# Kernel tuning notes

Measured on AMD Instinct MI355X. Metric: run time of the kernel, lower is better.

The kernel has to match this reference:

```python
import jax, jax.numpy as jnp
import numpy as np

B, S, D = 2, 2048, 1024
E, K = 8, 2
H = 1792  # round_up(int(1024*5/3)=1706, 256)


def setup_inputs() -> dict:
    key = jax.random.key(0)
    k1, k2, k3, k4, k5 = jax.random.split(key, 5)
    scale = 0.02
    x = jax.random.normal(k1, (B, S, D), dtype=jnp.float32)
    gate_w = jax.random.normal(k2, (E, D), dtype=jnp.float32) * scale   # nn.Linear(D,E).weight
    w_gate = jax.random.normal(k3, (E, D, H), dtype=jnp.float32) * scale
    w_up = jax.random.normal(k4, (E, D, H), dtype=jnp.float32) * scale
    w_down = jax.random.normal(k5, (E, H, D), dtype=jnp.float32) * scale
    return {"x": x, "gate_w": gate_w, "w_gate": w_gate, "w_up": w_up, "w_down": w_down}


def reference(x, gate_w, w_gate, w_up, w_down):
    b, s, d = x.shape
    x_flat = x.reshape(-1, d)                      # [T, D]
    # Gate computed in bf16 (torch autocast) then cast back to f32.
    logits = (x_flat.astype(jnp.bfloat16) @ gate_w.T.astype(jnp.bfloat16)).astype(jnp.float32)  # [T, E]
    topk_w, topk_idx = jax.lax.top_k(logits, K)    # [T, K]
    topk_w = jax.nn.softmax(topk_w, axis=-1)
    probs = jax.nn.softmax(logits, axis=-1)        # [T, E]
    mean_probs = probs.mean(0)                     # [E]
    load_balance_loss = E * jnp.sum(mean_probs ** 2)
    # Per-token combine weight for each expert (equivalent to sort/split/index_add combine).
    combine = jnp.sum(jax.nn.one_hot(topk_idx, E, dtype=x_flat.dtype) * topk_w[..., None], axis=1)  # [T, E]
    out = jnp.zeros_like(x_flat)
    for e in range(E):  # fixed small expert loop; math identical to grouped dispatch
        g = x_flat @ w_gate[e]                     # [T, H]
        u = x_flat @ w_up[e]                       # [T, H]
        y = (jax.nn.silu(g) * u) @ w_down[e]       # [T, D]
        out = out + y * combine[:, e:e + 1]
    return out.reshape(b, s, d), load_balance_loss, mean_probs
```

## Files before the change

### kernel.cpp

```cpp
#include <hip/hip_runtime.h>
#include <stdint.h>

#define TT 4096
#define DD 1024
#define EE 8
#define HH 1792
#define MP 10240
#define MT256 40
#define MT128 80

typedef __attribute__((ext_vector_type(8))) short short8;
typedef __attribute__((ext_vector_type(4))) short short4v;
typedef __attribute__((ext_vector_type(4))) float f32x4;

static __device__ __forceinline__ unsigned short f2bf(float f) {
  union { float f; uint32_t u; } v; v.f = f;
  return (unsigned short)((v.u + 0x7fffu + ((v.u >> 16) & 1u)) >> 16);
}
static __device__ __forceinline__ float bf2f(unsigned short h) {
  union { uint32_t u; float f; } v; v.u = ((uint32_t)h) << 16;
  return v.f;
}

static __device__ __forceinline__ void gll16(const void* g, const void* l) {
  __builtin_amdgcn_global_load_lds(
      (const __attribute__((address_space(1))) unsigned int*)g,
      (__attribute__((address_space(3))) unsigned int*)l, 16, 0, 0);
}

__global__ __launch_bounds__(256) void prep_weights(
    const float* __restrict__ w_gate, const float* __restrict__ w_up,
    const float* __restrict__ w_down, unsigned short* __restrict__ wguT,
    unsigned short* __restrict__ wdT) {
  __shared__ float L0[64][65];
  __shared__ float L1[64][65];
  const int tid = threadIdx.x;
  const int lr = tid >> 2, lc = (tid & 3) * 16;
  int bid = blockIdx.x;
  if (bid < 3584) {
    const int e = bid / 448, r = bid % 448;
    const int bx = r / 28, by = r % 28;
    const size_t so = (size_t)e * DD * HH + (size_t)(bx * 64) * HH + by * 64;
    const float* g = w_gate + so;
    const float* u = w_up + so;
#pragma unroll
    for (int q = 0; q < 4; ++q) {
      const f32x4 vg = *(const f32x4*)(g + (size_t)lr * HH + lc + 4 * q);
      const f32x4 vu = *(const f32x4*)(u + (size_t)lr * HH + lc + 4 * q);
#pragma unroll
      for (int j = 0; j < 4; ++j) {
        L0[lr][lc + 4 * q + j] = vg[j];
        L1[lr][lc + 4 * q + j] = vu[j];
      }
    }
    __syncthreads();
    unsigned short b0[16], b1[16];
#pragma unroll
    for (int q = 0; q < 16; ++q) {
      b0[q] = f2bf(L0[lc + q][lr]);
      b1[q] = f2bf(L1[lc + q][lr]);
    }
    const int h = by * 64 + lr;
    const int pg = (h >> 4) * 32 + (h & 15);
    unsigned short* dst = wguT + (size_t)e * 2 * HH * DD + (size_t)bx * 64 + lc;
    *(short8*)(dst + (size_t)pg * DD) = *(const short8*)&b0[0];
    *(short8*)(dst + (size_t)pg * DD + 8) = *(const short8*)&b0[8];
    *(short8*)(dst + (size_t)(pg + 16) * DD) = *(const short8*)&b1[0];
    *(short8*)(dst + (size_t)(pg + 16) * DD + 8) = *(const short8*)&b1[8];
  } else {
    bid -= 3584;
    const int e = bid / 448, r = bid % 448;
    const int bx = r / 16, by = r % 16;
    const float* src = w_down + (size_t)e * HH * DD + (size_t)(bx * 64) * DD + by * 64;
#pragma unroll
    for (int q = 0; q < 4; ++q) {
      const f32x4 v = *(const f32x4*)(src + (size_t)lr * DD + lc + 4 * q);
#pragma unroll
      for (int j = 0; j < 4; ++j) L0[lr][lc + 4 * q + j] = v[j];
    }
    __syncthreads();
    unsigned short b0[16];
#pragma unroll
    for (int q = 0; q < 16; ++q) b0[q] = f2bf(L0[lc + q][lr]);
    const int d = by * 64 + lr;
    unsigned short* dst = wdT + (size_t)e * DD * HH + (size_t)d * HH + bx * 64 + lc;
    *(short8*)(dst) = *(const short8*)&b0[0];
    *(short8*)(dst + 8) = *(const short8*)&b0[8];
  }
}

__global__ __launch_bounds__(256) void gate_kernel(
    const float* __restrict__ x, const float* __restrict__ gw,
    float* __restrict__ combine, float* __restrict__ probs, int2* __restrict__ topk) {
  const int lane = threadIdx.x & 63;
  const int wave = threadIdx.x >> 6;
  const int t = blockIdx.x * 4 + wave;
  const float* xr = x + (size_t)t * DD;
  float acc[EE];
#pragma unroll
  for (int e = 0; e < EE; ++e) acc[e] = 0.f;
  for (int i = 0; i < DD / 64; ++i) {
    const int d = i * 64 + lane;
    const float xv = bf2f(f2bf(xr[d]));
#pragma unroll
    for (int e = 0; e < EE; ++e)
      acc[e] += xv * bf2f(f2bf(gw[e * DD + d]));
  }
#pragma unroll
  for (int e = 0; e < EE; ++e) {
#pragma unroll
    for (int off = 32; off > 0; off >>= 1)
      acc[e] += __shfl_xor(acc[e], off, 64);
  }
  if (lane == 0) {
    float lg[EE];
#pragma unroll
    for (int e = 0; e < EE; ++e) lg[e] = bf2f(f2bf(acc[e]));
    float m1 = -1e30f, m2 = -1e30f; int i1 = 0, i2 = 0;
#pragma unroll
    for (int e = 0; e < EE; ++e) {
      const float v = lg[e];
      if (v > m1) { m2 = m1; i2 = i1; m1 = v; i1 = e; }
      else if (v > m2) { m2 = v; i2 = e; }
    }
    const float e2 = expf(m2 - m1);
    const float w1 = 1.f / (1.f + e2);
    const float w2 = e2 * w1;
    float cb[EE];
#pragma unroll
    for (int e = 0; e < EE; ++e) cb[e] = 0.f;
    cb[i1] = w1; cb[i2] += w2;
    float p[EE]; float s = 0.f;
#pragma unroll
    for (int e = 0; e < EE; ++e) { p[e] = expf(lg[e] - m1); s += p[e]; }
    const float inv = 1.f / s;
#pragma unroll
    for (int e = 0; e < EE; ++e) {
      combine[(size_t)t * EE + e] = cb[e];
      probs[(size_t)t * EE + e] = p[e] * inv;
    }
    topk[t] = make_int2(i1, i2);
  }
}

__global__ __launch_bounds__(256) void reduce_kernel(
    const float* __restrict__ probs, float* __restrict__ tail) {
  const int tid = threadIdx.x;
  const int lane = tid & 63, wave = tid >> 6;
  float acc[EE];
#pragma unroll
  for (int e = 0; e < EE; ++e) acc[e] = 0.f;
  for (int t = tid; t < TT; t += 256) {
#pragma unroll
    for (int e = 0; e < EE; ++e) acc[e] += probs[(size_t)t * EE + e];
  }
#pragma unroll
  for (int e = 0; e < EE; ++e) {
#pragma unroll
    for (int off = 32; off > 0; off >>= 1)
      acc[e] += __shfl_xor(acc[e], off, 64);
  }
  __shared__ float sm[4][EE];
  if (lane == 0) {
#pragma unroll
    for (int e = 0; e < EE; ++e) sm[wave][e] = acc[e];
  }
  __syncthreads();
  if (tid == 0) {
    float loss = 0.f;
#pragma unroll
    for (int e = 0; e < EE; ++e) {
      const float m = (sm[0][e] + sm[1][e] + sm[2][e] + sm[3][e]) * (1.f / TT);
      tail[1 + e] = m;
      loss += m * m;
    }
    tail[0] = (float)EE * loss;
  }
}

__global__ __launch_bounds__(512) void route_kernel(
    const int2* __restrict__ topk, const float* __restrict__ combine,
    int* __restrict__ tok_list, float* __restrict__ wt_list,
    int* __restrict__ tab256, int* __restrict__ tab128) {
  const int lane = threadIdx.x & 63;
  const int e = threadIdx.x >> 6;
  __shared__ int cnts[EE], offs[EE];
  int cnt = 0;
  for (int i = 0; i < TT / 64; ++i) {
    const int2 k2 = topk[i * 64 + lane];
    cnt += __popcll(__ballot(k2.x == e || k2.y == e));
  }
  if (lane == 0) cnts[e] = cnt;
  __syncthreads();
  if (threadIdx.x == 0) {
    int off = 0, n256 = 0, n128 = 0;
    for (int f = 0; f < EE; ++f) {
      offs[f] = off;
      const int pc = (cnts[f] + 255) & ~255;
      for (int j = 0; j < (pc >> 8); ++j) {
        tab256[2 * n256] = f; tab256[2 * n256 + 1] = off + 256 * j; ++n256;
      }
      for (int j = 0; j < (pc >> 7); ++j) {
        tab128[2 * n128] = f; tab128[2 * n128 + 1] = off + 128 * j; ++n128;
      }
      off += pc;
    }
    for (; n256 < MT256; ++n256) { tab256[2 * n256] = -1; tab256[2 * n256 + 1] = 0; }
    for (; n128 < MT128; ++n128) { tab128[2 * n128] = -1; tab128[2 * n128 + 1] = 0; }
  }
  __syncthreads();
  int pos = offs[e];
  for (int i = 0; i < TT / 64; ++i) {
    const int t = i * 64 + lane;
    const int2 k2 = topk[t];
    const bool sel = (k2.x == e || k2.y == e);
    const unsigned long long m = __ballot(sel);
    if (sel) {
      const int p = pos + __popcll(m & ((1ull << lane) - 1ull));
      tok_list[p] = t;
      wt_list[p] = combine[(size_t)t * EE + e];
    }
    pos += __popcll(m);
  }
  const int pc = (cnt + 255) & ~255;
  for (int s = cnt + lane; s < pc; s += 64) {
    tok_list[offs[e] + s] = 0;
    wt_list[offs[e] + s] = 0.f;
  }
}

__global__ __launch_bounds__(256) void gather_x(
    const float* __restrict__ x, const int* __restrict__ tok_list,
    const int* __restrict__ tab256, unsigned short* __restrict__ xg) {
  const int e = tab256[2 * blockIdx.x];
  if (e < 0) return;
  const int row0 = tab256[2 * blockIdx.x + 1] + blockIdx.y * 16;
  const int tid = threadIdx.x;
#pragma unroll
  for (int i = 0; i < 16; ++i) {
    const int row = row0 + i;
    const int tok = tok_list[row];
    const f32x4 v = *(const f32x4*)(x + (size_t)tok * DD + tid * 4);
    unsigned short b[4] = {f2bf(v[0]), f2bf(v[1]), f2bf(v[2]), f2bf(v[3])};
    *(short4v*)(xg + (size_t)row * DD + tid * 4) = *(const short4v*)b;
  }
}

template <int MODE>
__global__ __launch_bounds__(256, 3) void gemm128(
    const unsigned short* __restrict__ Ab, const unsigned short* __restrict__ Bb,
    const int* __restrict__ tab, const int* __restrict__ tok_list,
    const float* __restrict__ wt_list, unsigned short* __restrict__ act,
    float* __restrict__ out) {
  constexpr int K   = (MODE == 0) ? DD : HH;
  constexpr int NBR = (MODE == 0) ? 2 * HH : DD;
  constexpr int NNT = NBR / 128;
  __shared__ unsigned short As[128 * 64];
  __shared__ unsigned short Bs[128 * 64];

  const int nwg = gridDim.x;
  const int wgid = (blockIdx.x & 7) * (nwg >> 3) + (blockIdx.x >> 3);
  const int mt = wgid / NNT, nt = wgid % NNT;
  const int e = tab[2 * mt];
  if (e < 0) return;
  const int row0 = tab[2 * mt + 1];
  const int n0 = nt * 128;

  const int tid = threadIdx.x, lane = tid & 63, wave = tid >> 6;
  const int wm = (wave >> 1) * 64, wn = (wave & 1) * 64;
  const int fr = lane & 15, hi = lane >> 4;

  const unsigned short* At = Ab + (size_t)row0 * K;
  const unsigned short* Bt = Bb + ((size_t)e * NBR + n0) * K;

  const int srel = tid * 16;
  const int srow0 = srel >> 7;
  const int sch = (srel >> 4) & 7;

  f32x4 acc[4][4];
#pragma unroll
  for (int i = 0; i < 4; ++i)
#pragma unroll
    for (int j = 0; j < 4; ++j) acc[i][j] = (f32x4){0.f, 0.f, 0.f, 0.f};

  for (int k0 = 0; k0 < K; k0 += 64) {
#pragma unroll
    for (int q = 0; q < 4; ++q) {
      const int row = q * 32 + srow0;
      gll16(At + (size_t)row * K + k0 + ((sch ^ (row & 7)) << 3),
            (const char*)As + q * 4096 + srel);
    }
#pragma unroll
    for (int q = 0; q < 4; ++q) {
      const int row = q * 32 + srow0;
      gll16(Bt + (size_t)row * K + k0 + ((sch ^ (row & 7)) << 3),
            (const char*)Bs + q * 4096 + srel);
    }
    __syncthreads();
#pragma unroll
    for (int kc = 0; kc < 2; ++kc) {
      short8 a[4], b[4];
#pragma unroll
      for (int i = 0; i < 4; ++i) {
        const int row = wm + i * 16 + fr;
        a[i] = *(const short8*)((const char*)As + ((row * 128 + kc * 64 + hi * 16) ^ ((row & 7) << 4)));
      }
#pragma unroll
      for (int j = 0; j < 4; ++j) {
        const int row = wn + j * 16 + fr;
        b[j] = *(const short8*)((const char*)Bs + ((row * 128 + kc * 64 + hi * 16) ^ ((row & 7) << 4)));
      }
#pragma unroll
      for (int i = 0; i < 4; ++i)
#pragma unroll
        for (int j = 0; j < 4; ++j)
          acc[i][j] = __builtin_amdgcn_mfma_f32_16x16x32_bf16(a[i], b[j], acc[i][j], 0, 0, 0);
    }
    __syncthreads();
  }

  const int r4 = hi * 4;
  if constexpr (MODE == 0) {
#pragma unroll
    for (int i = 0; i < 4; ++i)
#pragma unroll
      for (int r = 0; r < 4; ++r) {
        const int row = row0 + wm + i * 16 + r4 + r;
#pragma unroll
        for (int jj = 0; jj < 2; ++jj) {
          const float g = acc[i][2 * jj][r], u = acc[i][2 * jj + 1][r];
          const int nb = n0 + wn + jj * 32;
          const int h = ((nb >> 5) << 4) + fr;
          act[(size_t)row * HH + h] = f2bf((g / (1.f + expf(-g))) * u);
        }
      }
  } else {
#pragma unroll
    for (int i = 0; i < 4; ++i)
#pragma unroll
      for (int r = 0; r < 4; ++r) {
        const int rl = row0 + wm + i * 16 + r4 + r;
        const int tok = tok_list[rl];
        const float wt = wt_list[rl];
        if (wt != 0.f) {
#pragma unroll
          for (int j = 0; j < 4; ++j)
            unsafeAtomicAdd(&out[(size_t)tok * DD + n0 + wn + j * 16 + fr],
                            acc[i][j][r] * wt);
        }
      }
  }
}

extern "C" void kernel_launch(void* const* d_in, const int* in_sizes, int n_in,
                              void* d_out, int out_size, void* d_ws, size_t ws_size,
                              hipStream_t stream) {
  const float* x      = (const float*)d_in[0];
  const float* gw     = (const float*)d_in[1];
  const float* w_gate = (const float*)d_in[2];
  const float* w_up   = (const float*)d_in[3];
  const float* w_down = (const float*)d_in[4];
  float* out = (float*)d_out;
  float* tail = out + (size_t)TT * DD;

  char* w = (char*)d_ws;
  size_t o = 0;
  auto carve = [&](size_t bytes) { char* p = w + o; o += (bytes + 255) & ~255ull; return p; };
  unsigned short* wguT = (unsigned short*)carve((size_t)EE * 2 * HH * DD * 2);
  unsigned short* wdT  = (unsigned short*)carve((size_t)EE * DD * HH * 2);
  unsigned short* xg   = (unsigned short*)carve((size_t)MP * DD * 2);
  unsigned short* act  = (unsigned short*)carve((size_t)MP * HH * 2);
  float* combine = (float*)carve((size_t)TT * EE * 4);
  float* probs   = (float*)carve((size_t)TT * EE * 4);
  int2* topk     = (int2*)carve((size_t)TT * 8);
  int* tok_list  = (int*)carve((size_t)MP * 4);
  float* wt_list = (float*)carve((size_t)MP * 4);
  int* tab256    = (int*)carve((size_t)MT256 * 8);
  int* tab128    = (int*)carve((size_t)MT128 * 8);

  hipMemsetAsync(out, 0, (size_t)TT * DD * sizeof(float), stream);

  prep_weights<<<7168, 256, 0, stream>>>(w_gate, w_up, w_down, wguT, wdT);

  gate_kernel<<<TT / 4, 256, 0, stream>>>(x, gw, combine, probs, topk);
  reduce_kernel<<<1, 256, 0, stream>>>(probs, tail);
  route_kernel<<<1, 512, 0, stream>>>(topk, combine, tok_list, wt_list, tab256, tab128);
  gather_x<<<dim3(MT256, 16), 256, 0, stream>>>(x, tok_list, tab256, xg);

  gemm128<0><<<MT128 * 28, 256, 0, stream>>>(xg, wguT, tab128, nullptr, nullptr, act, nullptr);
  gemm128<1><<<MT128 * 8, 256, 0, stream>>>(act, wdT, tab128, tok_list, wt_list, nullptr, out);
}
```

Before: 263.3 us.

## Pad expert segments to 128 rows, fold loss reduction into routing

```diff
diff --git a/kernel.cpp b/kernel.cpp
--- a/kernel.cpp
+++ b/kernel.cpp
@@ -6,7 +6,6 @@
 #define EE 8
 #define HH 1792
 #define MP 10240
-#define MT256 40
 #define MT128 80
 
 typedef __attribute__((ext_vector_type(8))) short short8;
@@ -143,48 +142,14 @@
   }
 }
 
-__global__ __launch_bounds__(256) void reduce_kernel(
-    const float* __restrict__ probs, float* __restrict__ tail) {
-  const int tid = threadIdx.x;
-  const int lane = tid & 63, wave = tid >> 6;
-  float acc[EE];
-#pragma unroll
-  for (int e = 0; e < EE; ++e) acc[e] = 0.f;
-  for (int t = tid; t < TT; t += 256) {
-#pragma unroll
-    for (int e = 0; e < EE; ++e) acc[e] += probs[(size_t)t * EE + e];
-  }
-#pragma unroll
-  for (int e = 0; e < EE; ++e) {
-#pragma unroll
-    for (int off = 32; off > 0; off >>= 1)
-      acc[e] += __shfl_xor(acc[e], off, 64);
-  }
-  __shared__ float sm[4][EE];
-  if (lane == 0) {
-#pragma unroll
-    for (int e = 0; e < EE; ++e) sm[wave][e] = acc[e];
-  }
-  __syncthreads();
-  if (tid == 0) {
-    float loss = 0.f;
-#pragma unroll
-    for (int e = 0; e < EE; ++e) {
-      const float m = (sm[0][e] + sm[1][e] + sm[2][e] + sm[3][e]) * (1.f / TT);
-      tail[1 + e] = m;
-      loss += m * m;
-    }
-    tail[0] = (float)EE * loss;
-  }
-}
-
 __global__ __launch_bounds__(512) void route_kernel(
     const int2* __restrict__ topk, const float* __restrict__ combine,
-    int* __restrict__ tok_list, float* __restrict__ wt_list,
-    int* __restrict__ tab256, int* __restrict__ tab128) {
+    const float* __restrict__ probs, int* __restrict__ tok_list,
+    float* __restrict__ wt_list, int* __restrict__ tab128, float* __restrict__ tail) {
   const int lane = threadIdx.x & 63;
   const int e = threadIdx.x >> 6;
   __shared__ int cnts[EE], offs[EE];
+  __shared__ float sm[EE];
   int cnt = 0;
   for (int i = 0; i < TT / 64; ++i) {
     const int2 k2 = topk[i * 64 + lane];
@@ -193,19 +158,15 @@
   if (lane == 0) cnts[e] = cnt;
   __syncthreads();
   if (threadIdx.x == 0) {
-    int off = 0, n256 = 0, n128 = 0;
+    int off = 0, n128 = 0;
     for (int f = 0; f < EE; ++f) {
       offs[f] = off;
-      const int pc = (cnts[f] + 255) & ~255;
-      for (int j = 0; j < (pc >> 8); ++j) {
-        tab256[2 * n256] = f; tab256[2 * n256 + 1] = off + 256 * j; ++n256;
-      }
+      const int pc = (cnts[f] + 127) & ~127;
       for (int j = 0; j < (pc >> 7); ++j) {
         tab128[2 * n128] = f; tab128[2 * n128 + 1] = off + 128 * j; ++n128;
       }
       off += pc;
     }
-    for (; n256 < MT256; ++n256) { tab256[2 * n256] = -1; tab256[2 * n256 + 1] = 0; }
     for (; n128 < MT128; ++n128) { tab128[2 * n128] = -1; tab128[2 * n128 + 1] = 0; }
   }
   __syncthreads();
@@ -222,19 +183,35 @@
     }
     pos += __popcll(m);
   }
-  const int pc = (cnt + 255) & ~255;
+  const int pc = (cnt + 127) & ~127;
   for (int s = cnt + lane; s < pc; s += 64) {
     tok_list[offs[e] + s] = 0;
     wt_list[offs[e] + s] = 0.f;
   }
+  float racc = 0.f;
+  for (int t = lane; t < TT; t += 64) racc += probs[(size_t)t * EE + e];
+#pragma unroll
+  for (int off = 32; off > 0; off >>= 1) racc += __shfl_xor(racc, off, 64);
+  if (lane == 0) {
+    const float m = racc * (1.f / TT);
+    sm[e] = m;
+    tail[1 + e] = m;
+  }
+  __syncthreads();
+  if (threadIdx.x == 0) {
+    float loss = 0.f;
+#pragma unroll
+    for (int f = 0; f < EE; ++f) loss += sm[f] * sm[f];
+    tail[0] = (float)EE * loss;
+  }
 }
 
 __global__ __launch_bounds__(256) void gather_x(
     const float* __restrict__ x, const int* __restrict__ tok_list,
-    const int* __restrict__ tab256, unsigned short* __restrict__ xg) {
-  const int e = tab256[2 * blockIdx.x];
+    const int* __restrict__ tab128, unsigned short* __restrict__ xg) {
+  const int e = tab128[2 * blockIdx.x];
   if (e < 0) return;
-  const int row0 = tab256[2 * blockIdx.x + 1] + blockIdx.y * 16;
+  const int row0 = tab128[2 * blockIdx.x + 1] + blockIdx.y * 16;
   const int tid = threadIdx.x;
 #pragma unroll
   for (int i = 0; i < 16; ++i) {
@@ -247,7 +224,7 @@
 }
 
 template <int MODE>
-__global__ __launch_bounds__(256, 3) void gemm128(
+__global__ __launch_bounds__(256, 5) void gemm128(
     const unsigned short* __restrict__ Ab, const unsigned short* __restrict__ Bb,
     const int* __restrict__ tab, const int* __restrict__ tok_list,
     const float* __restrict__ wt_list, unsigned short* __restrict__ act,
@@ -375,7 +352,6 @@
   int2* topk     = (int2*)carve((size_t)TT * 8);
   int* tok_list  = (int*)carve((size_t)MP * 4);
   float* wt_list = (float*)carve((size_t)MP * 4);
-  int* tab256    = (int*)carve((size_t)MT256 * 8);
   int* tab128    = (int*)carve((size_t)MT128 * 8);
 
   hipMemsetAsync(out, 0, (size_t)TT * DD * sizeof(float), stream);
@@ -383,9 +359,8 @@
   prep_weights<<<7168, 256, 0, stream>>>(w_gate, w_up, w_down, wguT, wdT);
 
   gate_kernel<<<TT / 4, 256, 0, stream>>>(x, gw, combine, probs, topk);
-  reduce_kernel<<<1, 256, 0, stream>>>(probs, tail);
-  route_kernel<<<1, 512, 0, stream>>>(topk, combine, tok_list, wt_list, tab256, tab128);
-  gather_x<<<dim3(MT256, 16), 256, 0, stream>>>(x, tok_list, tab256, xg);
+  route_kernel<<<1, 512, 0, stream>>>(topk, combine, probs, tok_list, wt_list, tab128, tail);
+  gather_x<<<dim3(MT128, 8), 256, 0, stream>>>(x, tok_list, tab128, xg);
 
   gemm128<0><<<MT128 * 28, 256, 0, stream>>>(xg, wguT, tab128, nullptr, nullptr, act, nullptr);
   gemm128<1><<<MT128 * 8, 256, 0, stream>>>(act, wdT, tab128, tok_list, wt_list, nullptr, out);
```

Result: slower. 446.3 us (+69.5%).
